# Performance work log

Hardware: AMD Instinct MI355X
Metric: run time of the kernel (lower is better)

## Reference

```python
import jax, jax.numpy as jnp
import numpy as np

N = 200000      # nodes
E = 200000      # edges per direction
IN = 256        # in_dim
HID = 256       # hidden_dim
HEADS = 4
C = HID // HEADS  # 64 per-head channels
OUT = 128
EPS = 1e-5      # LayerNorm eps (torch default)


def _ln(x, g, b):
    m = jnp.mean(x, axis=-1, keepdims=True)
    v = jnp.mean(jnp.square(x - m), axis=-1, keepdims=True)
    return (x - m) / jnp.sqrt(v + EPS) * g + b


def _gat(x, W, att_src, att_dst, bias, edge_index):
    """PyG GATConv (default args: add_self_loops=True, negative_slope=0.2, concat heads)."""
    n = x.shape[0]
    loops = jnp.arange(n, dtype=edge_index.dtype)
    ei = jnp.concatenate([edge_index, jnp.stack([loops, loops])], axis=1)
    src, dst = ei[0], ei[1]
    h = (x @ W).reshape(n, HEADS, C)                      # [N,H,C]
    a_src = jnp.sum(h * att_src, axis=-1)                 # [N,H]
    a_dst = jnp.sum(h * att_dst, axis=-1)                 # [N,H]
    e = jax.nn.leaky_relu(a_src[src] + a_dst[dst], 0.2)   # [E+N,H]
    m = jax.ops.segment_max(e, dst, num_segments=n)       # per-dst softmax max
    ex = jnp.exp(e - m[dst])
    denom = jax.ops.segment_sum(ex, dst, num_segments=n)
    alpha = ex / denom[dst]                               # [E+N,H]
    out = jax.ops.segment_sum(h[src] * alpha[..., None], dst, num_segments=n)
    return out.reshape(n, HEADS * C) + bias


def setup_inputs() -> dict:
    key = jax.random.key(0)
    ks = jax.random.split(key, 20)
    w = lambda k, s, sc=0.05: jax.random.normal(k, s, jnp.float32) * sc
    return {
        "x": jax.random.normal(ks[0], (N, IN), jnp.float32),
        "edge_index_bu": jax.random.randint(ks[1], (2, E), 0, N, jnp.int32),
        "edge_index_td": jax.random.randint(ks[2], (2, E), 0, N, jnp.int32),
        "Wp": w(ks[3], (IN, HID)), "bp": jnp.zeros((HID,), jnp.float32),
        "W_bu": w(ks[4], (HID, HID)), "asrc_bu": w(ks[5], (HEADS, C)),
        "adst_bu": w(ks[6], (HEADS, C)), "bias_bu": jnp.zeros((HID,), jnp.float32),
        "W_td": w(ks[7], (HID, HID)), "asrc_td": w(ks[8], (HEADS, C)),
        "adst_td": w(ks[9], (HEADS, C)), "bias_td": jnp.zeros((HID,), jnp.float32),
        "Wf": w(ks[10], (2 * HID, OUT)), "bf": jnp.zeros((OUT,), jnp.float32),
        "g_bu": jnp.ones((HID,), jnp.float32), "b_bu": jnp.zeros((HID,), jnp.float32),
        "g_td": jnp.ones((HID,), jnp.float32), "b_td": jnp.zeros((HID,), jnp.float32),
        "g_out": jnp.ones((OUT,), jnp.float32), "b_out": jnp.zeros((OUT,), jnp.float32),
    }


def reference(x, edge_index_bu, edge_index_td, Wp, bp,
              W_bu, asrc_bu, adst_bu, bias_bu,
              W_td, asrc_td, adst_td, bias_td,
              Wf, bf, g_bu, b_bu, g_td, b_td, g_out, b_out):
    h = jax.nn.relu(x @ Wp + bp)  # dropout is identity in eval
    x_bu = jax.nn.relu(_ln(_gat(h, W_bu, asrc_bu, adst_bu, bias_bu, edge_index_bu), g_bu, b_bu))
    x_td = jax.nn.relu(_ln(_gat(h, W_td, asrc_td, adst_td, bias_td, edge_index_td), g_td, b_td))
    out = jnp.concatenate([x_bu, x_td], axis=-1) @ Wf + bf
    out = _ln(out, g_out, b_out)
    nrm = jnp.sqrt(jnp.sum(jnp.square(out), axis=-1, keepdims=True))
    return out / jnp.maximum(nrm, 1e-12)
```

## Files before the change

### kernel.cpp

```cpp
#include <hip/hip_runtime.h>
#include <hip/hip_bf16.h>
#include <stdint.h>


typedef __attribute__((ext_vector_type(8))) short bf16x8;
typedef __attribute__((ext_vector_type(4))) short bf16x4;
typedef __attribute__((ext_vector_type(4))) float f32x4;

#define HID 256

__device__ __forceinline__ float red16(float v) {
    #pragma unroll
    for (int o = 1; o < 16; o <<= 1) v += __shfl_xor(v, o, 64);
    return v;
}
__device__ __forceinline__ float bf2f(short s) {
    return __uint_as_float(((unsigned)(unsigned short)s) << 16);
}

__device__ __forceinline__ void gload_lds16(const void* g, void* l) {
    __builtin_amdgcn_global_load_lds(
        reinterpret_cast<const __attribute__((address_space(1))) uint32_t*>(
            reinterpret_cast<uintptr_t>(g)),
        reinterpret_cast<__attribute__((address_space(3))) uint32_t*>(
            reinterpret_cast<uintptr_t>(l)),
        16, 0, 0);
}

__global__ void transpose_w(const float* __restrict__ W,
                            __hip_bfloat16* __restrict__ Wt, int KI, int KO) {
    int idx = blockIdx.x * 256 + threadIdx.x;
    if (idx >= KI * KO) return;
    int k = idx / KO, j = idx % KO;
    Wt[(long)j * KI + k] = __float2bfloat16(W[idx]);
}

template<int BN, int MODE, int CVT>
__global__ __launch_bounds__(512) void gemm_tiled(
    const float* __restrict__ Af, const __hip_bfloat16* __restrict__ Ab, int lda,
    const __hip_bfloat16* __restrict__ Bt, int KI,
    const float* __restrict__ bias, int doRelu,
    __hip_bfloat16* __restrict__ outB, int ldcB, int colOff,
    float* __restrict__ outF,
    const float* __restrict__ asrcW, const float* __restrict__ adstW,
    float* __restrict__ aS, float* __restrict__ aD,
    const float* __restrict__ gw, const float* __restrict__ bw, int N) {

    constexpr int WN = BN / 64;
    constexpr int WM = 8 / WN;
    constexpr int MR = (128 / WM) / 16;

    __shared__ __align__(16) __hip_bfloat16 sA[2][128 * 32];
    __shared__ __align__(16) __hip_bfloat16 sB[2][BN * 32];
    __shared__ float sRed[MODE == 2 ? 128 * 4 : 4];
    __shared__ float sN2[MODE == 2 ? 128 * 2 : 2];

    int tid = threadIdx.x;
    int wv = tid >> 6, ln = tid & 63;
    int m = ln & 15, q = ln >> 4;
    long row0 = (long)blockIdx.x * 128;
    int wr = (wv / WN) * (128 / WM);
    int wc = (wv % WN) * 64;

    f32x4 acc[MR][4];
    #pragma unroll
    for (int mi = 0; mi < MR; ++mi)
        #pragma unroll
        for (int t = 0; t < 4; ++t) acc[mi][t] = (f32x4){0.f, 0.f, 0.f, 0.f};

    int oA = tid * 16;
    long rowA = row0 + (oA >> 6);
    if (rowA >= N) rowA = N - 1;
    int kel = (oA & 63) >> 1;
    long aBase = rowA * (long)lda + kel;

    auto stage = [&](int buf, int k0) {
        if constexpr (CVT) {
            const float* src = Af + aBase + k0;
            f32x4 fa0 = *(const f32x4*)src;
            f32x4 fa1 = *(const f32x4*)(src + 4);
            __hip_bfloat16 t8[8];
            t8[0] = __float2bfloat16(fa0[0]); t8[1] = __float2bfloat16(fa0[1]);
            t8[2] = __float2bfloat16(fa0[2]); t8[3] = __float2bfloat16(fa0[3]);
            t8[4] = __float2bfloat16(fa1[0]); t8[5] = __float2bfloat16(fa1[1]);
            t8[6] = __float2bfloat16(fa1[2]); t8[7] = __float2bfloat16(fa1[3]);
            *(bf16x8*)((char*)sA[buf] + oA) = *(const bf16x8*)t8;
        } else {
            gload_lds16(Ab + aBase + k0, (char*)sA[buf] + oA);
        }
        #pragma unroll
        for (int j = 0; j < BN / 128; ++j) {
            int o = j * 8192 + tid * 16;
            const __hip_bfloat16* src = Bt + (long)(o >> 6) * KI + k0 + ((o & 63) >> 1);
            gload_lds16(src, (char*)sB[buf] + o);
        }
    };

    stage(0, 0);
    __syncthreads();
    int cur = 0;
    for (int k0 = 0; k0 < KI; k0 += 32) {
        if (k0 + 32 < KI) stage(cur ^ 1, k0 + 32);

        bf16x8 af[MR], bfr[4];
        #pragma unroll
        for (int mi = 0; mi < MR; ++mi)
            af[mi] = *(const bf16x8*)((const char*)sA[cur] + ((wr + mi * 16 + m) << 6) + q * 16);
        #pragma unroll
        for (int t = 0; t < 4; ++t)
            bfr[t] = *(const bf16x8*)((const char*)sB[cur] + ((wc + t * 16 + m) << 6) + q * 16);
        #pragma unroll
        for (int mi = 0; mi < MR; ++mi)
            #pragma unroll
            for (int t = 0; t < 4; ++t)
                acc[mi][t] = __builtin_amdgcn_mfma_f32_16x16x32_bf16(af[mi], bfr[t],
                                                                     acc[mi][t], 0, 0, 0);
        __syncthreads();
        cur ^= 1;
    }

    if constexpr (MODE != 2) {
        #pragma unroll
        for (int mi = 0; mi < MR; ++mi) {
            #pragma unroll
            for (int t = 0; t < 4; ++t) {
                int col = wc + t * 16 + m;
                float bv = bias ? bias[col] : 0.f;
                #pragma unroll
                for (int r = 0; r < 4; ++r) {
                    long row = row0 + wr + mi * 16 + q * 4 + r;
                    if (row < N) {
                        float v = acc[mi][t][r] + bv;
                        if (doRelu) v = fmaxf(v, 0.f);
                        outB[row * ldcB + colOff + col] = __float2bfloat16(v);
                    }
                }
            }
        }
    }

    if constexpr (MODE == 1) {
        int h = wc >> 6;
        f32x4 sw, dw;
        #pragma unroll
        for (int t = 0; t < 4; ++t) {
            sw[t] = asrcW[wc + t * 16 + m];
            dw[t] = adstW[wc + t * 16 + m];
        }
        #pragma unroll
        for (int mi = 0; mi < MR; ++mi) {
            #pragma unroll
            for (int r = 0; r < 4; ++r) {
                float ps = acc[mi][0][r] * sw[0] + acc[mi][1][r] * sw[1]
                         + acc[mi][2][r] * sw[2] + acc[mi][3][r] * sw[3];
                float pd = acc[mi][0][r] * dw[0] + acc[mi][1][r] * dw[1]
                         + acc[mi][2][r] * dw[2] + acc[mi][3][r] * dw[3];
                ps = red16(ps); pd = red16(pd);
                long row = row0 + wr + mi * 16 + q * 4 + r;
                if (m == 0 && row < N) {
                    aS[row * 4 + h] = ps;
                    aD[row * 4 + h] = pd;
                }
            }
        }
    }

    if constexpr (MODE == 2) {
        float vv[MR][4][4];
        float gcol[4], bcol[4];
        #pragma unroll
        for (int t = 0; t < 4; ++t) {
            int col = wc + t * 16 + m;
            float bb = bias[col];
            gcol[t] = gw[col]; bcol[t] = bw[col];
            #pragma unroll
            for (int mi = 0; mi < MR; ++mi)
                #pragma unroll
                for (int r = 0; r < 4; ++r) vv[mi][t][r] = acc[mi][t][r] + bb;
        }
        int wcid = wc >> 6;
        #pragma unroll
        for (int mi = 0; mi < MR; ++mi) {
            #pragma unroll
            for (int r = 0; r < 4; ++r) {
                float s1 = vv[mi][0][r] + vv[mi][1][r] + vv[mi][2][r] + vv[mi][3][r];
                float s2 = vv[mi][0][r] * vv[mi][0][r] + vv[mi][1][r] * vv[mi][1][r]
                         + vv[mi][2][r] * vv[mi][2][r] + vv[mi][3][r] * vv[mi][3][r];
                s1 = red16(s1); s2 = red16(s2);
                if (m == 0) {
                    int lrow = wr + mi * 16 + q * 4 + r;
                    sRed[lrow * 4 + wcid * 2 + 0] = s1;
                    sRed[lrow * 4 + wcid * 2 + 1] = s2;
                }
            }
        }
        __syncthreads();
        #pragma unroll
        for (int mi = 0; mi < MR; ++mi) {
            #pragma unroll
            for (int r = 0; r < 4; ++r) {
                int lrow = wr + mi * 16 + q * 4 + r;
                float S1 = sRed[lrow * 4 + 0] + sRed[lrow * 4 + 2];
                float S2 = sRed[lrow * 4 + 1] + sRed[lrow * 4 + 3];
                float mean = S1 * (1.f / 128.f);
                float var = S2 * (1.f / 128.f) - mean * mean;
                float inv = rsqrtf(fmaxf(var, 0.f) + 1e-5f);
                float n2 = 0.f;
                #pragma unroll
                for (int t = 0; t < 4; ++t) {
                    float y = (vv[mi][t][r] - mean) * inv * gcol[t] + bcol[t];
                    vv[mi][t][r] = y;
                    n2 += y * y;
                }
                n2 = red16(n2);
                if (m == 0) sN2[lrow * 2 + wcid] = n2;
            }
        }
        __syncthreads();
        #pragma unroll
        for (int mi = 0; mi < MR; ++mi) {
            #pragma unroll
            for (int r = 0; r < 4; ++r) {
                int lrow = wr + mi * 16 + q * 4 + r;
                long row = row0 + lrow;
                float nrm = sqrtf(sN2[lrow * 2] + sN2[lrow * 2 + 1]);
                float sc = 1.f / fmaxf(nrm, 1e-12f);
                if (row < N) {
                    #pragma unroll
                    for (int t = 0; t < 4; ++t)
                        outF[row * 128 + wc + t * 16 + m] = vv[mi][t][r] * sc;
                }
            }
        }
    }
}

__global__ __launch_bounds__(256) void hist_dst(const int* __restrict__ ei, int E,
                                                int* __restrict__ cnt) {
    int e = blockIdx.x * 256 + threadIdx.x;
    if (e < E) atomicAdd(&cnt[ei[E + e]], 1);
}

__global__ __launch_bounds__(256) void scan1(const int* __restrict__ cnt,
                                             int* __restrict__ offpart,
                                             int* __restrict__ bsum, int n) {
    int t = threadIdx.x, i = blockIdx.x * 256 + t;
    int lane = t & 63, w = t >> 6;
    int v = (i < n) ? cnt[i] : 0;
    int inc = v;
    #pragma unroll
    for (int o = 1; o < 64; o <<= 1) {
        int u = __shfl_up(inc, o, 64);
        if (lane >= o) inc += u;
    }
    __shared__ int wsum[4];
    if (lane == 63) wsum[w] = inc;
    __syncthreads();
    int wadd = 0;
    #pragma unroll
    for (int k = 0; k < 4; ++k) if (k < w) wadd += wsum[k];
    if (i < n) offpart[i] = inc - v + wadd;
    if (t == 255) bsum[blockIdx.x] = inc + wadd;
}

__global__ __launch_bounds__(256) void scan2(const int* __restrict__ bsum,
                                             int* __restrict__ btot, int nb) {
    int t = threadIdx.x, lane = t & 63, w = t >> 6;
    int loc[4]; int s = 0;
    #pragma unroll
    for (int k = 0; k < 4; ++k) {
        int idx = t * 4 + k;
        int v = (idx < nb) ? bsum[idx] : 0;
        loc[k] = s; s += v;
    }
    int inc = s;
    #pragma unroll
    for (int o = 1; o < 64; o <<= 1) {
        int u = __shfl_up(inc, o, 64);
        if (lane >= o) inc += u;
    }
    __shared__ int wsum[4];
    if (lane == 63) wsum[w] = inc;
    __syncthreads();
    int wadd = 0;
    #pragma unroll
    for (int k = 0; k < 4; ++k) if (k < w) wadd += wsum[k];
    int excl = inc - s + wadd;
    #pragma unroll
    for (int k = 0; k < 4; ++k) {
        int idx = t * 4 + k;
        if (idx < nb) btot[idx] = excl + loc[k];
    }
}

__global__ __launch_bounds__(256) void finalize_off(const int* __restrict__ offpart,
                                                    const int* __restrict__ btot,
                                                    int* __restrict__ off, int n, int E) {
    int i = blockIdx.x * 256 + threadIdx.x;
    if (i < n) off[i] = offpart[i] + btot[i >> 8];
    if (i == 0) off[n] = E;
}

__global__ __launch_bounds__(256) void scatter_src(const int* __restrict__ ei, int E,
                                                   const int* __restrict__ off,
                                                   int* __restrict__ cur,
                                                   int* __restrict__ esrc) {
    int e = blockIdx.x * 256 + threadIdx.x;
    if (e >= E) return;
    int d = ei[E + e];
    int pos = off[d] + atomicAdd(&cur[d], 1);
    esrc[pos] = ei[e];
}

__global__ __launch_bounds__(256) void att_alpha(
    const int* __restrict__ off, const int* __restrict__ esrc,
    const float* __restrict__ a_s, const float* __restrict__ a_d,
    float* __restrict__ alpha_self, float* __restrict__ alpha_e, int N) {
    int d = blockIdx.x * 256 + threadIdx.x;
    if (d >= N) return;
    int beg = off[d], end = off[d + 1];
    f32x4 adv = *(const f32x4*)(a_d + 4 * (long)d);
    f32x4 asd = *(const f32x4*)(a_s + 4 * (long)d);
    float es[4], m[4];
    #pragma unroll
    for (int h = 0; h < 4; ++h) {
        float e = asd[h] + adv[h]; e = e > 0.f ? e : 0.2f * e;
        es[h] = e; m[h] = e;
    }
    for (int j = beg; j < end; ++j) {
        int s = esrc[j];
        f32x4 asv = *(const f32x4*)(a_s + 4 * (long)s);
        #pragma unroll
        for (int h = 0; h < 4; ++h) {
            float e = asv[h] + adv[h]; e = e > 0.f ? e : 0.2f * e;
            m[h] = fmaxf(m[h], e);
        }
    }
    float sum[4];
    #pragma unroll
    for (int h = 0; h < 4; ++h) sum[h] = __expf(es[h] - m[h]);
    for (int j = beg; j < end; ++j) {
        int s = esrc[j];
        f32x4 asv = *(const f32x4*)(a_s + 4 * (long)s);
        #pragma unroll
        for (int h = 0; h < 4; ++h) {
            float e = asv[h] + adv[h]; e = e > 0.f ? e : 0.2f * e;
            sum[h] += __expf(e - m[h]);
        }
    }
    float rs[4];
    #pragma unroll
    for (int h = 0; h < 4; ++h) rs[h] = 1.f / sum[h];
    f32x4 sa;
    #pragma unroll
    for (int h = 0; h < 4; ++h) sa[h] = __expf(es[h] - m[h]) * rs[h];
    *(f32x4*)(alpha_self + 4 * (long)d) = sa;
    for (int j = beg; j < end; ++j) {
        int s = esrc[j];
        f32x4 asv = *(const f32x4*)(a_s + 4 * (long)s);
        f32x4 av;
        #pragma unroll
        for (int h = 0; h < 4; ++h) {
            float e = asv[h] + adv[h]; e = e > 0.f ? e : 0.2f * e;
            av[h] = __expf(e - m[h]) * rs[h];
        }
        *(f32x4*)(alpha_e + 4 * (long)j) = av;
    }
}

__global__ __launch_bounds__(256) void gat_gather(
    const int* __restrict__ off, const int* __restrict__ esrc,
    const float* __restrict__ alpha_self, const float* __restrict__ alpha_e,
    const __hip_bfloat16* __restrict__ hw, int dirOff,
    const float* __restrict__ bias, const float* __restrict__ g,
    const float* __restrict__ b,
    __hip_bfloat16* __restrict__ out, int N) {
    int tid = threadIdx.x;
    int lane = tid & 63;
    int grp = lane >> 4, li = lane & 15;
    long d = (long)blockIdx.x * 16 + (tid >> 6) * 4 + grp;
    if (d >= N) return;
    int beg = off[d], end = off[d + 1];
    int head = li >> 2;
    int c0 = li * 16;
    float acc[16];
    {
        float a = alpha_self[4 * d + head];
        const __hip_bfloat16* r = hw + d * 512 + dirOff + c0;
        bf16x8 h0 = *(const bf16x8*)r;
        bf16x8 h1 = *(const bf16x8*)(r + 8);
        #pragma unroll
        for (int k = 0; k < 8; ++k) {
            acc[k] = a * bf2f(h0[k]);
            acc[8 + k] = a * bf2f(h1[k]);
        }
    }
    for (int j = beg; j < end; ++j) {
        int s = esrc[j];
        float a = alpha_e[4 * (long)j + head];
        const __hip_bfloat16* r = hw + (long)s * 512 + dirOff + c0;
        bf16x8 h0 = *(const bf16x8*)r;
        bf16x8 h1 = *(const bf16x8*)(r + 8);
        #pragma unroll
        for (int k = 0; k < 8; ++k) {
            acc[k] += a * bf2f(h0[k]);
            acc[8 + k] += a * bf2f(h1[k]);
        }
    }
    float s1 = 0.f, s2 = 0.f;
    #pragma unroll
    for (int k = 0; k < 16; k += 4) {
        f32x4 bi = *(const f32x4*)(bias + c0 + k);
        #pragma unroll
        for (int u = 0; u < 4; ++u) {
            float v = acc[k + u] + bi[u];
            acc[k + u] = v;
            s1 += v; s2 += v * v;
        }
    }
    #pragma unroll
    for (int o = 1; o < 16; o <<= 1) {
        s1 += __shfl_xor(s1, o, 64);
        s2 += __shfl_xor(s2, o, 64);
    }
    float mean = s1 * (1.f / 256.f);
    float var = s2 * (1.f / 256.f) - mean * mean;
    float inv = rsqrtf(fmaxf(var, 0.f) + 1e-5f);
    __hip_bfloat16 o16[16];
    #pragma unroll
    for (int k = 0; k < 16; k += 4) {
        f32x4 gv = *(const f32x4*)(g + c0 + k);
        f32x4 bv = *(const f32x4*)(b + c0 + k);
        #pragma unroll
        for (int u = 0; u < 4; ++u) {
            float y = (acc[k + u] - mean) * inv * gv[u] + bv[u];
            o16[k + u] = __float2bfloat16(fmaxf(y, 0.f));
        }
    }
    __hip_bfloat16* orow = out + d * 512 + dirOff + c0;
    *(bf16x8*)orow = *(const bf16x8*)o16;
    *(bf16x8*)(orow + 8) = *(const bf16x8*)(o16 + 8);
}

extern "C" void kernel_launch(void* const* d_in, const int* in_sizes, int n_in,
                              void* d_out, int out_size, void* d_ws, size_t ws_size,
                              hipStream_t stream) {
    const float* x      = (const float*)d_in[0];
    const int*   ei_bu  = (const int*)d_in[1];
    const int*   ei_td  = (const int*)d_in[2];
    const float* Wp     = (const float*)d_in[3];
    const float* bp     = (const float*)d_in[4];
    const float* W_bu   = (const float*)d_in[5];
    const float* asrc_bu= (const float*)d_in[6];
    const float* adst_bu= (const float*)d_in[7];
    const float* bias_bu= (const float*)d_in[8];
    const float* W_td   = (const float*)d_in[9];
    const float* asrc_td= (const float*)d_in[10];
    const float* adst_td= (const float*)d_in[11];
    const float* bias_td= (const float*)d_in[12];
    const float* Wf     = (const float*)d_in[13];
    const float* bfv    = (const float*)d_in[14];
    const float* g_bu   = (const float*)d_in[15];
    const float* b_bu   = (const float*)d_in[16];
    const float* g_td   = (const float*)d_in[17];
    const float* b_td   = (const float*)d_in[18];
    const float* g_out  = (const float*)d_in[19];
    const float* b_out  = (const float*)d_in[20];

    const int N = in_sizes[0] / HID;
    const int E = in_sizes[1] / 2;

    char* ws = (char*)d_ws;
    size_t off0 = 0;
    auto take = [&](size_t bytes) -> char* {
        char* p = ws + off0;
        off0 += (bytes + 255) & ~(size_t)255;
        return p;
    };
    __hip_bfloat16* h_buf = (__hip_bfloat16*)take((size_t)N * 256 * 2);
    __hip_bfloat16* hwcat = (__hip_bfloat16*)take((size_t)N * 512 * 2);
    __hip_bfloat16* xcat  = (__hip_bfloat16*)take((size_t)N * 512 * 2);
    float* aS0   = (float*)take((size_t)N * 16);
    float* aD0   = (float*)take((size_t)N * 16);
    float* aS1   = (float*)take((size_t)N * 16);
    float* aD1   = (float*)take((size_t)N * 16);
    float* alsf  = (float*)take((size_t)N * 16);
    float* ale   = (float*)take((size_t)E * 16);
    int* cnt     = (int*)take((size_t)N * 4);
    int* cur     = (int*)take((size_t)N * 4);
    int* offpart = (int*)take((size_t)N * 4);
    int* offarr  = (int*)take((size_t)(N + 1) * 4);
    int* esrc    = (int*)take((size_t)E * 4);
    int* bsum    = (int*)take(1024 * 4);
    int* btot    = (int*)take(1024 * 4);
    __hip_bfloat16* Wpt  = (__hip_bfloat16*)take(256 * 256 * 2);
    __hip_bfloat16* Wcat = (__hip_bfloat16*)take(512 * 256 * 2);
    __hip_bfloat16* Wft  = (__hip_bfloat16*)take(128 * 512 * 2);

    transpose_w<<<(256 * 256 + 255) / 256, 256, 0, stream>>>(Wp, Wpt, 256, 256);
    transpose_w<<<(256 * 256 + 255) / 256, 256, 0, stream>>>(W_bu, Wcat, 256, 256);
    transpose_w<<<(256 * 256 + 255) / 256, 256, 0, stream>>>(W_td, Wcat + 256 * 256, 256, 256);
    transpose_w<<<(512 * 128 + 255) / 256, 256, 0, stream>>>(Wf, Wft, 512, 128);

    int gm = (N + 127) / 128;

    gemm_tiled<256, 0, 1><<<gm, 512, 0, stream>>>(
        x, nullptr, 256, Wpt, 256, bp, 1, h_buf, 256, 0, nullptr,
        nullptr, nullptr, nullptr, nullptr, nullptr, nullptr, N);

    gemm_tiled<256, 1, 0><<<gm, 512, 0, stream>>>(
        nullptr, h_buf, 256, Wcat, 256, nullptr, 0, hwcat, 512, 0, nullptr,
        asrc_bu, adst_bu, aS0, aD0, nullptr, nullptr, N);
    gemm_tiled<256, 1, 0><<<gm, 512, 0, stream>>>(
        nullptr, h_buf, 256, Wcat + 256 * 256, 256, nullptr, 0, hwcat, 512, 256, nullptr,
        asrc_td, adst_td, aS1, aD1, nullptr, nullptr, N);

    const int* eis[2] = {ei_bu, ei_td};
    const float* aSs[2] = {aS0, aS1};
    const float* aDs[2] = {aD0, aD1};
    const float* biases[2]= {bias_bu, bias_td};
    const float* gs[2]    = {g_bu, g_td};
    const float* bs[2]    = {b_bu, b_td};

    int egrid = (E + 255) / 256;
    int ngrid = (N + 255) / 256;
    int nb = (N + 255) / 256;
    for (int dir = 0; dir < 2; ++dir) {
        hipMemsetAsync(cnt, 0, (size_t)N * 8, stream);
        hist_dst<<<egrid, 256, 0, stream>>>(eis[dir], E, cnt);
        scan1<<<nb, 256, 0, stream>>>(cnt, offpart, bsum, N);
        scan2<<<1, 256, 0, stream>>>(bsum, btot, nb);
        finalize_off<<<ngrid, 256, 0, stream>>>(offpart, btot, offarr, N, E);
        scatter_src<<<egrid, 256, 0, stream>>>(eis[dir], E, offarr, cur, esrc);
        att_alpha<<<ngrid, 256, 0, stream>>>(offarr, esrc, aSs[dir], aDs[dir],
                                             alsf, ale, N);
        gat_gather<<<(N + 15) / 16, 256, 0, stream>>>(offarr, esrc, alsf, ale,
                                                      hwcat, dir * 256,
                                                      biases[dir], gs[dir], bs[dir],
                                                      xcat, N);
    }

    gemm_tiled<128, 2, 0><<<gm, 512, 0, stream>>>(
        nullptr, xcat, 512, Wft, 512, bfv, 0, nullptr, 128, 0, (float*)d_out,
        nullptr, nullptr, nullptr, nullptr, g_out, b_out, N);
}
```

Baseline: 892.7 us.

## Fuse both GAT direction projections into one 1024-thread GEMM kernel

Replaces the two per-direction GEMM launches (h @ W_bu, h @ W_td with attention-logit epilogues) with a single kernel using 1024 threads that computes all 512 output columns per 128-row tile. The A tile of h is loaded once into shared memory and reused for both directions, and the attention-score epilogue is selected per wave by column range. The new kernel drops double buffering and uses a single-stage load with two barriers per k-step, so load latency is less hidden. The refactored generic GEMM loses its MODE 1 path and gets an extra barrier in the MODE 2 epilogue.

```diff
diff --git a/kernel.cpp b/kernel.cpp
--- a/kernel.cpp
+++ b/kernel.cpp
@@ -42,8 +42,6 @@
     const float* __restrict__ bias, int doRelu,
     __hip_bfloat16* __restrict__ outB, int ldcB, int colOff,
     float* __restrict__ outF,
-    const float* __restrict__ asrcW, const float* __restrict__ adstW,
-    float* __restrict__ aS, float* __restrict__ aD,
     const float* __restrict__ gw, const float* __restrict__ bw, int N) {
 
     constexpr int WN = BN / 64;
@@ -96,25 +94,28 @@
         }
     };
 
+    auto compute = [&](int buf) {
+        bf16x8 af[MR], bfr[4];
+        #pragma unroll
+        for (int mi = 0; mi < MR; ++mi)
+            af[mi] = *(const bf16x8*)((const char*)sA[buf] + ((wr + mi * 16 + m) << 6) + q * 16);
+        #pragma unroll
+        for (int t = 0; t < 4; ++t)
+            bfr[t] = *(const bf16x8*)((const char*)sB[buf] + ((wc + t * 16 + m) << 6) + q * 16);
+        #pragma unroll
+        for (int mi = 0; mi < MR; ++mi)
+            #pragma unroll
+            for (int t = 0; t < 4; ++t)
+                acc[mi][t] = __builtin_amdgcn_mfma_f32_16x16x32_bf16(af[mi], bfr[t],
+                                                                     acc[mi][t], 0, 0, 0);
+    };
+
     stage(0, 0);
     __syncthreads();
     int cur = 0;
     for (int k0 = 0; k0 < KI; k0 += 32) {
         if (k0 + 32 < KI) stage(cur ^ 1, k0 + 32);
-
-        bf16x8 af[MR], bfr[4];
-        #pragma unroll
-        for (int mi = 0; mi < MR; ++mi)
-            af[mi] = *(const bf16x8*)((const char*)sA[cur] + ((wr + mi * 16 + m) << 6) + q * 16);
-        #pragma unroll
-        for (int t = 0; t < 4; ++t)
-            bfr[t] = *(const bf16x8*)((const char*)sB[cur] + ((wc + t * 16 + m) << 6) + q * 16);
-        #pragma unroll
-        for (int mi = 0; mi < MR; ++mi)
-            #pragma unroll
-            for (int t = 0; t < 4; ++t)
-                acc[mi][t] = __builtin_amdgcn_mfma_f32_16x16x32_bf16(af[mi], bfr[t],
-                                                                     acc[mi][t], 0, 0, 0);
+        compute(cur);
         __syncthreads();
         cur ^= 1;
     }
@@ -139,32 +140,6 @@
         }
     }
 
-    if constexpr (MODE == 1) {
-        int h = wc >> 6;
-        f32x4 sw, dw;
-        #pragma unroll
-        for (int t = 0; t < 4; ++t) {
-            sw[t] = asrcW[wc + t * 16 + m];
-            dw[t] = adstW[wc + t * 16 + m];
-        }
-        #pragma unroll
-        for (int mi = 0; mi < MR; ++mi) {
-            #pragma unroll
-            for (int r = 0; r < 4; ++r) {
-                float ps = acc[mi][0][r] * sw[0] + acc[mi][1][r] * sw[1]
-                         + acc[mi][2][r] * sw[2] + acc[mi][3][r] * sw[3];
-                float pd = acc[mi][0][r] * dw[0] + acc[mi][1][r] * dw[1]
-                         + acc[mi][2][r] * dw[2] + acc[mi][3][r] * dw[3];
-                ps = red16(ps); pd = red16(pd);
-                long row = row0 + wr + mi * 16 + q * 4 + r;
-                if (m == 0 && row < N) {
-                    aS[row * 4 + h] = ps;
-                    aD[row * 4 + h] = pd;
-                }
-            }
-        }
-    }
-
     if constexpr (MODE == 2) {
         float vv[MR][4][4];
         float gcol[4], bcol[4];
@@ -179,6 +154,7 @@
                 for (int r = 0; r < 4; ++r) vv[mi][t][r] = acc[mi][t][r] + bb;
         }
         int wcid = wc >> 6;
+        __syncthreads();
         #pragma unroll
         for (int mi = 0; mi < MR; ++mi) {
             #pragma unroll
@@ -230,6 +206,109 @@
                     for (int t = 0; t < 4; ++t)
                         outF[row * 128 + wc + t * 16 + m] = vv[mi][t][r] * sc;
                 }
+            }
+        }
+    }
+}
+
+__global__ __launch_bounds__(1024) void gemm_dir2(
+    const __hip_bfloat16* __restrict__ Ab,
+    const __hip_bfloat16* __restrict__ Bt,
+    const float* __restrict__ asrc0, const float* __restrict__ adst0,
+    const float* __restrict__ asrc1, const float* __restrict__ adst1,
+    float* __restrict__ aS0, float* __restrict__ aD0,
+    float* __restrict__ aS1, float* __restrict__ aD1,
+    __hip_bfloat16* __restrict__ outB, int N) {
+    constexpr int KI = 256;
+    __shared__ __align__(16) __hip_bfloat16 sA[128 * 32];
+    __shared__ __align__(16) __hip_bfloat16 sB[512 * 32];
+
+    int tid = threadIdx.x;
+    int wv = tid >> 6, ln = tid & 63;
+    int m = ln & 15, q = ln >> 4;
+    long row0 = (long)blockIdx.x * 128;
+    int wr = (wv >> 3) * 64;
+    int wc = (wv & 7) * 64;
+
+    f32x4 acc[4][4];
+    #pragma unroll
+    for (int mi = 0; mi < 4; ++mi)
+        #pragma unroll
+        for (int t = 0; t < 4; ++t) acc[mi][t] = (f32x4){0.f, 0.f, 0.f, 0.f};
+
+    int oA = (tid & 511) * 16;
+    long rowA = row0 + (oA >> 6);
+    if (rowA >= N) rowA = N - 1;
+    int kel = (oA & 63) >> 1;
+    long aBase = rowA * (long)KI + kel;
+    int oB0 = tid * 16;
+    int kelB = (oB0 & 63) >> 1;
+
+    for (int k0 = 0; k0 < KI; k0 += 32) {
+        __syncthreads();
+        if (tid < 512) gload_lds16(Ab + aBase + k0, (char*)sA + oA);
+        #pragma unroll
+        for (int j = 0; j < 2; ++j) {
+            int o = j * 16384 + oB0;
+            const __hip_bfloat16* src = Bt + (long)(o >> 6) * KI + k0 + ((o & 63) >> 1);
+            gload_lds16(src, (char*)sB + o);
+        }
+        __syncthreads();
+
+        bf16x8 af[4], bfr[4];
+        #pragma unroll
+        for (int mi = 0; mi < 4; ++mi)
+            af[mi] = *(const bf16x8*)((const char*)sA + ((wr + mi * 16 + m) << 6) + q * 16);
+        #pragma unroll
+        for (int t = 0; t < 4; ++t)
+            bfr[t] = *(const bf16x8*)((const char*)sB + ((wc + t * 16 + m) << 6) + q * 16);
+        #pragma unroll
+        for (int mi = 0; mi < 4; ++mi)
+            #pragma unroll
+            for (int t = 0; t < 4; ++t)
+                acc[mi][t] = __builtin_amdgcn_mfma_f32_16x16x32_bf16(af[mi], bfr[t],
+                                                                     acc[mi][t], 0, 0, 0);
+    }
+
+    #pragma unroll
+    for (int mi = 0; mi < 4; ++mi) {
+        #pragma unroll
+        for (int t = 0; t < 4; ++t) {
+            int col = wc + t * 16 + m;
+            #pragma unroll
+            for (int r = 0; r < 4; ++r) {
+                long row = row0 + wr + mi * 16 + q * 4 + r;
+                if (row < N) outB[row * 512 + col] = __float2bfloat16(acc[mi][t][r]);
+            }
+        }
+    }
+
+    int dir = wc >> 8;
+    int cc = wc & 255;
+    int h = cc >> 6;
+    const float* as_ = dir ? asrc1 : asrc0;
+    const float* ad_ = dir ? adst1 : adst0;
+    float* aS = dir ? aS1 : aS0;
+    float* aD = dir ? aD1 : aD0;
+    f32x4 sw, dw;
+    #pragma unroll
+    for (int t = 0; t < 4; ++t) {
+        sw[t] = as_[cc + t * 16 + m];
+        dw[t] = ad_[cc + t * 16 + m];
+    }
+    #pragma unroll
+    for (int mi = 0; mi < 4; ++mi) {
+        #pragma unroll
+        for (int r = 0; r < 4; ++r) {
+            float ps = acc[mi][0][r] * sw[0] + acc[mi][1][r] * sw[1]
+                     + acc[mi][2][r] * sw[2] + acc[mi][3][r] * sw[3];
+            float pd = acc[mi][0][r] * dw[0] + acc[mi][1][r] * dw[1]
+                     + acc[mi][2][r] * dw[2] + acc[mi][3][r] * dw[3];
+            ps = red16(ps); pd = red16(pd);
+            long row = row0 + wr + mi * 16 + q * 4 + r;
+            if (m == 0 && row < N) {
+                aS[row * 4 + h] = ps;
+                aD[row * 4 + h] = pd;
             }
         }
     }
@@ -506,14 +585,11 @@
 
     gemm_tiled<256, 0, 1><<<gm, 512, 0, stream>>>(
         x, nullptr, 256, Wpt, 256, bp, 1, h_buf, 256, 0, nullptr,
-        nullptr, nullptr, nullptr, nullptr, nullptr, nullptr, N);
-
-    gemm_tiled<256, 1, 0><<<gm, 512, 0, stream>>>(
-        nullptr, h_buf, 256, Wcat, 256, nullptr, 0, hwcat, 512, 0, nullptr,
-        asrc_bu, adst_bu, aS0, aD0, nullptr, nullptr, N);
-    gemm_tiled<256, 1, 0><<<gm, 512, 0, stream>>>(
-        nullptr, h_buf, 256, Wcat + 256 * 256, 256, nullptr, 0, hwcat, 512, 256, nullptr,
-        asrc_td, adst_td, aS1, aD1, nullptr, nullptr, N);
+        nullptr, nullptr, N);
+
+    gemm_dir2<<<gm, 1024, 0, stream>>>(
+        h_buf, Wcat, asrc_bu, adst_bu, asrc_td, adst_td,
+        aS0, aD0, aS1, aD1, hwcat, N);
 
     const int* eis[2] = {ei_bu, ei_td};
     const float* aSs[2] = {aS0, aS1};
@@ -542,5 +618,5 @@
 
     gemm_tiled<128, 2, 0><<<gm, 512, 0, stream>>>(
         nullptr, xcat, 512, Wft, 512, bfv, 0, nullptr, 128, 0, (float*)d_out,
-        nullptr, nullptr, nullptr, nullptr, g_out, b_out, N);
-}
+        g_out, b_out, N);
+}
```

Measured after the change: 871.0 us. 2.4% less time.
